# Optimization experiments

Hardware: AMD Instinct MI355X
Metric: run time of the kernel (lower is better)

## Reference

```python
import jax, jax.numpy as jnp
import numpy as np

K_MSG = 1024   # message length k (rows of G)
N_CODE = 2048  # codeword length n (cols of G)
B = 32768      # number of message blocks


def setup_inputs() -> dict:
    key = jax.random.key(0)
    kb, kg = jax.random.split(key)
    b = jax.random.randint(kb, (B, K_MSG), 0, 2, dtype=jnp.int32)
    G = jax.random.randint(kg, (K_MSG, N_CODE), 0, 2, dtype=jnp.int32)
    return {"b": b, "G": G}


def reference(b, G):
    # GF(2) linear block encode: c = (b @ G) mod 2
    # b: [num_blocks, k] bits (0/1), G: [k, n] generator matrix (0/1)
    b2 = b.astype(jnp.int32)
    G2 = G.astype(jnp.int32)
    c = jnp.mod(jnp.matmul(b2, G2), 2)  # [num_blocks, n]
    return c.astype(jnp.int32)
```

## Files before the change

kernel.cpp:

```cpp
#include <hip/hip_runtime.h>
#include <stdint.h>

typedef unsigned int u32;
typedef unsigned long long u64;
typedef int v4i  __attribute__((ext_vector_type(4)));
typedef int v16i __attribute__((ext_vector_type(16)));

#define K_MSG   1024
#define N_CODE  2048
#define NB      32768

__global__ void pack_gBF(const int* __restrict__ G, u32* __restrict__ bf) {
    int idx = blockIdx.x * blockDim.x + threadIdx.x;
    const int j  = idx & (N_CODE - 1);
    const int kq = idx >> 11;
    u32 p = 0;
#pragma unroll
    for (int i = 0; i < 4; ++i) {
        int v = G[(size_t)(kq * 4 + i) * N_CODE + j];
        p |= (u32)(v & 1) << (8 * i);
    }
    const int jb = j >> 5, jr = j & 31;
    const int kb = kq >> 3, hi = (kq >> 2) & 1, b4 = kq & 3;
    bf[(size_t)(jb * 32 + kb) * 256 + hi * 128 + jr * 4 + b4] = p;
}


#define MFMA_I8(va, vb, vc) __builtin_amdgcn_mfma_i32_32x32x32_i8(va, vb, vc, 0, 0, 0)

#define MFMA_SET(sfx) do {                              \
    acc[0][0] = MFMA_I8(a0##sfx, b0##sfx, acc[0][0]);   \
    acc[0][1] = MFMA_I8(a0##sfx, b1##sfx, acc[0][1]);   \
    acc[0][2] = MFMA_I8(a0##sfx, b2##sfx, acc[0][2]);   \
    acc[0][3] = MFMA_I8(a0##sfx, b3##sfx, acc[0][3]);   \
    acc[1][0] = MFMA_I8(a1##sfx, b0##sfx, acc[1][0]);   \
    acc[1][1] = MFMA_I8(a1##sfx, b1##sfx, acc[1][1]);   \
    acc[1][2] = MFMA_I8(a1##sfx, b2##sfx, acc[1][2]);   \
    acc[1][3] = MFMA_I8(a1##sfx, b3##sfx, acc[1][3]);   \
} while (0)

#define LOAD_SET(sfx, s_) do {                                      \
    int ao_ = lr * 1024 + ((((s_) * 32) + hi * 16) ^ axor);         \
    a0##sfx = *(const v4i*)(As + ao_);                              \
    a1##sfx = *(const v4i*)(As + ao_ + 32768);                      \
    b0##sfx = *(const v4i*)(bp0 + (size_t)(s_) * 1024);             \
    b1##sfx = *(const v4i*)(bp1 + (size_t)(s_) * 1024);             \
    b2##sfx = *(const v4i*)(bp2 + (size_t)(s_) * 1024);             \
    b3##sfx = *(const v4i*)(bp3 + (size_t)(s_) * 1024);             \
} while (0)

__global__ __launch_bounds__(256, 2) void gemm_all(const int* __restrict__ b,
                                                   const char* __restrict__ bf,
                                                   int* __restrict__ out) {
    __shared__ __align__(16) char As[64 * 1024];
    __shared__ u32 pk[2][64 * 16];

    const int t   = threadIdx.x;
    const int bid = blockIdx.x;
    const int m0  = ((bid & 7) * 64 + (bid >> 3)) * 64;

    const int w = t >> 6, lane = t & 63, lr = lane & 31, hi = lane >> 5;
    const int axor = (lr & 7) << 4;

    {
        const int* src = b + (size_t)m0 * K_MSG;
#pragma unroll 8
        for (int i = 0; i < 64; ++i) {
            int4 v = *(const int4*)(src + (size_t)i * K_MSG + t * 4);
            u32 p = (u32)(v.x & 1) | ((u32)(v.y & 1) << 8) |
                    ((u32)(v.z & 1) << 16) | ((u32)(v.w & 1) << 24);
            *(u32*)(As + i * 1024 + ((t * 4) ^ ((i & 7) << 4))) = p;
        }
    }
    __syncthreads();

#pragma unroll 1
    for (int pass = 0; pass < 4; ++pass) {
        const int cur = pass & 1;
        const char* bp0 = bf + ((size_t)pass * 16 + w * 4) * 32768 + lane * 16;
        const char* bp1 = bp0 + 32768;
        const char* bp2 = bp0 + 65536;
        const char* bp3 = bp0 + 98304;

        v16i acc[2][4] = {};
        v4i a0A, a1A, b0A, b1A, b2A, b3A;
        v4i a0B, a1B, b0B, b1B, b2B, b3B;
        v4i a0C, a1C, b0C, b1C, b2C, b3C;
        v4i a0D, a1D, b0D, b1D, b2D, b3D;

        LOAD_SET(A, 0);
        LOAD_SET(B, 1);
#pragma unroll 1
        for (int s = 0; s < 32; s += 4) {
            LOAD_SET(C, s + 2);
            LOAD_SET(D, s + 3);
            MFMA_SET(A);
            MFMA_SET(B);
            if (s + 4 < 32) {
                LOAD_SET(A, s + 4);
                LOAD_SET(B, s + 5);
            }
            MFMA_SET(C);
            MFMA_SET(D);
        }

#pragma unroll
        for (int mi = 0; mi < 2; ++mi) {
#pragma unroll
            for (int ni = 0; ni < 4; ++ni) {
                const int cbL = w * 4 + ni;
#pragma unroll
                for (int r = 0; r < 16; ++r) {
                    u64 m = __ballot((acc[mi][ni][r] & 1) != 0);
                    if ((lane & 31) == r) {
                        const int row = mi * 32 + (r & 3) + 8 * (r >> 2) + 4 * hi;
                        pk[cur][row * 16 + cbL] = (u32)(m >> (hi * 32));
                    }
                }
            }
        }
        __syncthreads();

        int* op = out + (size_t)m0 * N_CODE + pass * 512;
#pragma unroll 1
        for (int rr = 0; rr < 16; ++rr) {
            const int row = w * 16 + rr;
            const int sb  = (lane & 7) * 4;
            u32 p0 = pk[cur][row * 16 + (lane >> 3)];
            u32 p1 = pk[cur][row * 16 + 8 + (lane >> 3)];
            v4i v0, v1;
            v0.x = (int)((p0 >> (sb + 0)) & 1u);
            v0.y = (int)((p0 >> (sb + 1)) & 1u);
            v0.z = (int)((p0 >> (sb + 2)) & 1u);
            v0.w = (int)((p0 >> (sb + 3)) & 1u);
            v1.x = (int)((p1 >> (sb + 0)) & 1u);
            v1.y = (int)((p1 >> (sb + 1)) & 1u);
            v1.z = (int)((p1 >> (sb + 2)) & 1u);
            v1.w = (int)((p1 >> (sb + 3)) & 1u);
            int* dst = op + (size_t)row * N_CODE + lane * 4;
            *(v4i*)dst         = v0;
            *(v4i*)(dst + 256) = v1;
        }
    }
}

__global__ void encode_naive(const int* __restrict__ b, const int* __restrict__ G,
                             int* __restrict__ out) {
    size_t idx = (size_t)blockIdx.x * blockDim.x + threadIdx.x;
    size_t total = (size_t)NB * N_CODE;
    if (idx >= total) return;
    int i = (int)(idx / N_CODE);
    int j = (int)(idx % N_CODE);
    int acc = 0;
    for (int k = 0; k < K_MSG; ++k)
        acc ^= b[(size_t)i * K_MSG + k] & G[(size_t)k * N_CODE + j];
    out[idx] = acc & 1;
}

extern "C" void kernel_launch(void* const* d_in, const int* in_sizes, int n_in,
                              void* d_out, int out_size, void* d_ws, size_t ws_size,
                              hipStream_t stream) {
    const int* b = (const int*)d_in[0];
    const int* G = (const int*)d_in[1];
    int* out = (int*)d_out;

    const size_t bf_bytes = (size_t)N_CODE * K_MSG;

    if (ws_size < bf_bytes) {
        size_t total = (size_t)NB * N_CODE;
        encode_naive<<<(unsigned)((total + 255) / 256), 256, 0, stream>>>(b, G, out);
        return;
    }

    char* bf = (char*)d_ws;

    pack_gBF<<<2048, 256, 0, stream>>>(G, (u32*)bf);
    gemm_all<<<NB / 64, 256, 0, stream>>>(b, bf, out);
}
```

Baseline: 138.9 us.

## Overlap previous pass's output expansion and stores with current pass MFMA loop

Output bit-expansion and global stores for pass p-1 are now interleaved into the MFMA k-loop of pass p, two rows per iteration, using the double-buffered packed-bit shared memory. Only the final pass's rows are written after the loop. The goal is to hide the large int32 output write traffic behind matrix compute instead of serialising it after each pass. It relies on the single __syncthreads per pass to keep the ping-pong buffer safe, and it adds register pressure inside the main loop.

```diff
diff --git a/kernel.cpp b/kernel.cpp
--- a/kernel.cpp
+++ b/kernel.cpp
@@ -49,6 +49,24 @@
     b3##sfx = *(const v4i*)(bp3 + (size_t)(s_) * 1024);             \
 } while (0)
 
+#define EXPAND_ROW(pkp_, opp_, row_) do {                           \
+    const u32 p0_ = (pkp_)[(row_) * 16 + (lane >> 3)];              \
+    const u32 p1_ = (pkp_)[(row_) * 16 + 8 + (lane >> 3)];          \
+    const int sb_ = (lane & 7) * 4;                                 \
+    v4i v0_, v1_;                                                   \
+    v0_.x = (int)((p0_ >> (sb_ + 0)) & 1u);                         \
+    v0_.y = (int)((p0_ >> (sb_ + 1)) & 1u);                         \
+    v0_.z = (int)((p0_ >> (sb_ + 2)) & 1u);                         \
+    v0_.w = (int)((p0_ >> (sb_ + 3)) & 1u);                         \
+    v1_.x = (int)((p1_ >> (sb_ + 0)) & 1u);                         \
+    v1_.y = (int)((p1_ >> (sb_ + 1)) & 1u);                         \
+    v1_.z = (int)((p1_ >> (sb_ + 2)) & 1u);                         \
+    v1_.w = (int)((p1_ >> (sb_ + 3)) & 1u);                         \
+    int* dst_ = (opp_) + (size_t)(row_) * N_CODE + lane * 4;        \
+    *(v4i*)dst_         = v0_;                                      \
+    *(v4i*)(dst_ + 256) = v1_;                                      \
+} while (0)
+
 __global__ __launch_bounds__(256, 2) void gemm_all(const int* __restrict__ b,
                                                    const char* __restrict__ bf,
                                                    int* __restrict__ out) {
@@ -77,6 +95,9 @@
 #pragma unroll 1
     for (int pass = 0; pass < 4; ++pass) {
         const int cur = pass & 1;
+        const u32* pkp = pk[cur ^ 1];
+        int* opp = out + (size_t)m0 * N_CODE + (pass - 1) * 512;
+
         const char* bp0 = bf + ((size_t)pass * 16 + w * 4) * 32768 + lane * 16;
         const char* bp1 = bp0 + 32768;
         const char* bp2 = bp0 + 65536;
@@ -102,8 +123,14 @@
             }
             MFMA_SET(C);
             MFMA_SET(D);
+            if (pass > 0) {
+                const int row0 = w * 16 + (s >> 1);
+                EXPAND_ROW(pkp, opp, row0);
+                EXPAND_ROW(pkp, opp, row0 + 1);
+            }
         }
 
+        u32* pkc = pk[cur];
 #pragma unroll
         for (int mi = 0; mi < 2; ++mi) {
 #pragma unroll
@@ -114,32 +141,21 @@
                     u64 m = __ballot((acc[mi][ni][r] & 1) != 0);
                     if ((lane & 31) == r) {
                         const int row = mi * 32 + (r & 3) + 8 * (r >> 2) + 4 * hi;
-                        pk[cur][row * 16 + cbL] = (u32)(m >> (hi * 32));
+                        pkc[row * 16 + cbL] = (u32)(m >> (hi * 32));
                     }
                 }
             }
         }
         __syncthreads();
+    }
 
-        int* op = out + (size_t)m0 * N_CODE + pass * 512;
-#pragma unroll 1
+    {
+        const u32* pkp = pk[1];
+        int* opp = out + (size_t)m0 * N_CODE + 3 * 512;
+#pragma unroll 4
         for (int rr = 0; rr < 16; ++rr) {
             const int row = w * 16 + rr;
-            const int sb  = (lane & 7) * 4;
-            u32 p0 = pk[cur][row * 16 + (lane >> 3)];
-            u32 p1 = pk[cur][row * 16 + 8 + (lane >> 3)];
-            v4i v0, v1;
-            v0.x = (int)((p0 >> (sb + 0)) & 1u);
-            v0.y = (int)((p0 >> (sb + 1)) & 1u);
-            v0.z = (int)((p0 >> (sb + 2)) & 1u);
-            v0.w = (int)((p0 >> (sb + 3)) & 1u);
-            v1.x = (int)((p1 >> (sb + 0)) & 1u);
-            v1.y = (int)((p1 >> (sb + 1)) & 1u);
-            v1.z = (int)((p1 >> (sb + 2)) & 1u);
-            v1.w = (int)((p1 >> (sb + 3)) & 1u);
-            int* dst = op + (size_t)row * N_CODE + lane * 4;
-            *(v4i*)dst         = v0;
-            *(v4i*)(dst + 256) = v1;
+            EXPAND_ROW(pkp, opp, row);
         }
     }
 }
```

After: 134.6 us. 1.03x faster.
